# Kernel tuning notes

Hardware: AMD Instinct MI355X
Metric: run time of the kernel (lower is better)

## Reference

```python
import jax, jax.numpy as jnp
import numpy as np

B, S, IN, HID = 8, 2048, 1024, 1024

def setup_inputs() -> dict:
    key = jax.random.key(0)
    ks = jax.random.split(key, 6)
    scale = 1.0 / np.sqrt(IN + HID)
    return {
        "x": jax.random.normal(ks[0], (B, S, IN), dtype=jnp.float32),
        "h": jax.random.normal(ks[1], (B, S, HID), dtype=jnp.float32),
        "W1": jax.random.normal(ks[2], (HID, IN + HID), dtype=jnp.float32) * scale,
        "b1": jax.random.normal(ks[3], (HID,), dtype=jnp.float32) * scale,
        "W2": jax.random.normal(ks[4], (HID, IN + HID), dtype=jnp.float32) * scale,
        "b2": jax.random.normal(ks[5], (HID,), dtype=jnp.float32) * scale,
    }

def reference(x, h, W1, b1, W2, b2):
    # combined1 = cat(x, h) ; forget = sigmoid(Linear1(combined1))
    combined1 = jnp.concatenate((x, h), axis=2)          # [B,S,IN+HID]
    forget = jax.nn.sigmoid(jnp.einsum('bsf,hf->bsh', combined1, W1) + b1)
    interim_h = forget * h                                # [B,S,HID]
    combined2 = jnp.concatenate((x, interim_h), axis=2)   # [B,S,IN+HID]
    interim_o = jnp.tanh(jnp.einsum('bsf,hf->bsh', combined2, W2) + b2)
    output = (1.0 - forget) * h + forget * interim_o
    return (output, output)
```

## Files before the change

### kernel.cpp

```cpp
#include <hip/hip_runtime.h>
#include <stdint.h>


#define M_ROWS 16384
#define K_DIM  2048
#define N_DIM  1024

typedef float  f32x4  __attribute__((ext_vector_type(4)));
typedef __bf16 bf16x8 __attribute__((ext_vector_type(8)));
typedef unsigned short u16x8 __attribute__((ext_vector_type(8)));

typedef __attribute__((address_space(3))) void as3_void;
typedef __attribute__((address_space(1))) void as1_void;

__device__ __forceinline__ void gload_lds16(const unsigned short* g, void* lds) {
    __builtin_amdgcn_global_load_lds((const as1_void*)g, (as3_void*)lds, 16, 0, 0);
}

__device__ __forceinline__ unsigned short f2bf(float f) {
    union { float f; unsigned u; } v; v.f = f;
    unsigned r = 0x7FFFu + ((v.u >> 16) & 1u);
    return (unsigned short)((v.u + r) >> 16);
}


__global__ void pack_A(const float* __restrict__ x, const float* __restrict__ h,
                       unsigned short* __restrict__ Abf) {
    size_t t = (size_t)blockIdx.x * blockDim.x + threadIdx.x;
    size_t e = t * 8;
    int row = (int)(e >> 11);
    int col = (int)(e & 2047);
    const float* src = (col < 1024) ? (x + (size_t)row * 1024 + col)
                                    : (h + (size_t)row * 1024 + (col - 1024));
    f32x4 v0 = ((const f32x4*)src)[0];
    f32x4 v1 = ((const f32x4*)src)[1];
    u16x8 o;
    o[0] = f2bf(v0[0]); o[1] = f2bf(v0[1]); o[2] = f2bf(v0[2]); o[3] = f2bf(v0[3]);
    o[4] = f2bf(v1[0]); o[5] = f2bf(v1[1]); o[6] = f2bf(v1[2]); o[7] = f2bf(v1[3]);
    *(u16x8*)(Abf + e) = o;
}

__global__ void pack_W(const float* __restrict__ W1, const float* __restrict__ W2,
                       unsigned short* __restrict__ W1b, unsigned short* __restrict__ W2b) {
    size_t t = (size_t)blockIdx.x * blockDim.x + threadIdx.x;
    size_t e = t * 8;
    int which = (int)(e >> 21);
    size_t e2 = e & ((1u << 21) - 1);
    const float* src = (which ? W2 : W1) + e2;
    unsigned short* dst = (which ? W2b : W1b) + e2;
    f32x4 v0 = ((const f32x4*)src)[0];
    f32x4 v1 = ((const f32x4*)src)[1];
    u16x8 o;
    o[0] = f2bf(v0[0]); o[1] = f2bf(v0[1]); o[2] = f2bf(v0[2]); o[3] = f2bf(v0[3]);
    o[4] = f2bf(v1[0]); o[5] = f2bf(v1[1]); o[6] = f2bf(v1[2]); o[7] = f2bf(v1[3]);
    *(u16x8*)dst = o;
}


#define NT (K_DIM / 32)

__global__ __launch_bounds__(256) void gemm1(
        const unsigned short* __restrict__ Abf,
        const unsigned short* __restrict__ Wb,
        const float* __restrict__ bias,
        const float* __restrict__ h,
        float* Fout,
        unsigned short* __restrict__ H2)
{
    __shared__ unsigned short As[2][4096];
    __shared__ unsigned short Bs[2][4096];

    int bid = blockIdx.x;
    int tn = bid & 7, tm = bid >> 3;
    int m0 = tm * 128, n0 = tn * 128;

    int t = threadIdx.x, wave = t >> 6;
    int lane = t & 63;
    int wr = wave >> 1, wc = wave & 1;
    int fr = lane & 15, fq = lane >> 4;
    int sRow = t >> 2, sCol = (t & 3) * 8;

    const unsigned short* aBase = Abf + (size_t)(m0 + sRow) * K_DIM + sCol;
    const unsigned short* bBase = Wb  + (size_t)(n0 + sRow) * K_DIM + sCol;
    int ldsW = wave * 1024;

#define STAGE1(bufi, k0s)                                              \
    do {                                                               \
        char* AsB = (char*)As[bufi];  char* BsB = (char*)Bs[bufi];     \
        gload_lds16(aBase + (k0s),                AsB + ldsW);         \
        gload_lds16(aBase + 64 * K_DIM + (k0s),   AsB + 4096 + ldsW);  \
        gload_lds16(bBase + (k0s),                BsB + ldsW);         \
        gload_lds16(bBase + 64 * K_DIM + (k0s),   BsB + 4096 + ldsW);  \
    } while (0)

    f32x4 acc[4][4] = {};

    STAGE1(0, 0);
    __syncthreads();

    int cur = 0;
    for (int ti = 0; ti < NT; ++ti) {
        if (ti + 1 < NT) STAGE1(cur ^ 1, (ti + 1) * 32);
        bf16x8 af[4], bfr[4];
#pragma unroll
        for (int i = 0; i < 4; i++) {
            af[i]  = *(const bf16x8*)&As[cur][(wr * 64 + i * 16 + fr) * 32 + fq * 8];
            bfr[i] = *(const bf16x8*)&Bs[cur][(wc * 64 + i * 16 + fr) * 32 + fq * 8];
        }
        __builtin_amdgcn_s_setprio(1);
#pragma unroll
        for (int mi = 0; mi < 4; mi++)
#pragma unroll
            for (int ni = 0; ni < 4; ni++)
                acc[mi][ni] = __builtin_amdgcn_mfma_f32_16x16x32_bf16(
                                  af[mi], bfr[ni], acc[mi][ni], 0, 0, 0);
        __builtin_amdgcn_s_setprio(0);
        __syncthreads();
        cur ^= 1;
    }
#undef STAGE1

    int rowBase = m0 + wr * 64 + fq * 4;
    int colBase = n0 + wc * 64 + fr;
#pragma unroll
    for (int mi = 0; mi < 4; mi++) {
#pragma unroll
        for (int ni = 0; ni < 4; ni++) {
            int col = colBase + ni * 16;
            float b = bias[col];
#pragma unroll
            for (int j = 0; j < 4; j++) {
                int row = rowBase + mi * 16 + j;
                size_t idx = (size_t)row * N_DIM + col;
                float c = acc[mi][ni][j] + b;
                float f = 1.0f / (1.0f + expf(-c));
                Fout[idx] = f;
                float hv = h[idx];
                H2[idx] = f2bf(f * hv);
            }
        }
    }
}

__global__ __launch_bounds__(256) void gemm2(
        const unsigned short* __restrict__ Abf,
        const unsigned short* __restrict__ H2,
        const unsigned short* __restrict__ Wb,
        const float* __restrict__ bias,
        const float* __restrict__ h,
        float* Fout,
        float* Out2)
{
    __shared__ unsigned short As[2][4096];
    __shared__ unsigned short Bs[2][4096];

    int bid = blockIdx.x;
    int tn = bid & 7, tm = bid >> 3;
    int m0 = tm * 128, n0 = tn * 128;

    int t = threadIdx.x, wave = t >> 6;
    int lane = t & 63;
    int wr = wave >> 1, wc = wave & 1;
    int fr = lane & 15, fq = lane >> 4;
    int sRow = t >> 2, sCol = (t & 3) * 8;

    const unsigned short* aBase1 = Abf + (size_t)(m0 + sRow) * K_DIM + sCol;
    const unsigned short* aBase2 = H2  + (size_t)(m0 + sRow) * N_DIM + sCol;
    const unsigned short* bBase  = Wb  + (size_t)(n0 + sRow) * K_DIM + sCol;
    int ldsW = wave * 1024;

#define STAGE2(bufi, k0s)                                                   \
    do {                                                                    \
        char* AsB = (char*)As[bufi];  char* BsB = (char*)Bs[bufi];          \
        if ((k0s) < 1024) {                                                 \
            gload_lds16(aBase1 + (k0s),               AsB + ldsW);          \
            gload_lds16(aBase1 + 64 * K_DIM + (k0s),  AsB + 4096 + ldsW);   \
        } else {                                                            \
            int kk = (k0s) - 1024;                                          \
            gload_lds16(aBase2 + kk,                  AsB + ldsW);          \
            gload_lds16(aBase2 + 64 * N_DIM + kk,     AsB + 4096 + ldsW);   \
        }                                                                   \
        gload_lds16(bBase + (k0s),                BsB + ldsW);              \
        gload_lds16(bBase + 64 * K_DIM + (k0s),   BsB + 4096 + ldsW);       \
    } while (0)

    f32x4 acc[4][4] = {};

    STAGE2(0, 0);
    __syncthreads();

    int cur = 0;
    for (int ti = 0; ti < NT; ++ti) {
        if (ti + 1 < NT) STAGE2(cur ^ 1, (ti + 1) * 32);
        bf16x8 af[4], bfr[4];
#pragma unroll
        for (int i = 0; i < 4; i++) {
            af[i]  = *(const bf16x8*)&As[cur][(wr * 64 + i * 16 + fr) * 32 + fq * 8];
            bfr[i] = *(const bf16x8*)&Bs[cur][(wc * 64 + i * 16 + fr) * 32 + fq * 8];
        }
        __builtin_amdgcn_s_setprio(1);
#pragma unroll
        for (int mi = 0; mi < 4; mi++)
#pragma unroll
            for (int ni = 0; ni < 4; ni++)
                acc[mi][ni] = __builtin_amdgcn_mfma_f32_16x16x32_bf16(
                                  af[mi], bfr[ni], acc[mi][ni], 0, 0, 0);
        __builtin_amdgcn_s_setprio(0);
        __syncthreads();
        cur ^= 1;
    }
#undef STAGE2

    int rowBase = m0 + wr * 64 + fq * 4;
    int colBase = n0 + wc * 64 + fr;
#pragma unroll
    for (int mi = 0; mi < 4; mi++) {
#pragma unroll
        for (int ni = 0; ni < 4; ni++) {
            int col = colBase + ni * 16;
            float b = bias[col];
#pragma unroll
            for (int j = 0; j < 4; j++) {
                int row = rowBase + mi * 16 + j;
                size_t idx = (size_t)row * N_DIM + col;
                float c = acc[mi][ni][j] + b;
                float o = tanhf(c);
                float f = Fout[idx];
                float hv = h[idx];
                float out = fmaf(f, o - hv, hv);
                Fout[idx] = out;
                Out2[idx] = out;
            }
        }
    }
}


extern "C" void kernel_launch(void* const* d_in, const int* in_sizes, int n_in,
                              void* d_out, int out_size, void* d_ws, size_t ws_size,
                              hipStream_t stream) {
    const float* x  = (const float*)d_in[0];
    const float* h  = (const float*)d_in[1];
    const float* W1 = (const float*)d_in[2];
    const float* b1 = (const float*)d_in[3];
    const float* W2 = (const float*)d_in[4];
    const float* b2 = (const float*)d_in[5];
    float* out = (float*)d_out;
    float* out2 = out + (size_t)M_ROWS * N_DIM;

    unsigned short* Abf = (unsigned short*)d_ws;
    unsigned short* H2  = (unsigned short*)((char*)d_ws + 67108864);
    unsigned short* W1b = (unsigned short*)((char*)d_ws + 100663296);
    unsigned short* W2b = (unsigned short*)((char*)d_ws + 104857600);

    pack_A<<<16384, 256, 0, stream>>>(x, h, Abf);
    pack_W<<<2048, 256, 0, stream>>>(W1, W2, W1b, W2b);
    gemm1<<<1024, 256, 0, stream>>>(Abf, W1b, b1, h, out, H2);
    gemm2<<<1024, 256, 0, stream>>>(Abf, H2, W2b, b2, h, out, out2);
}
```

Measured before the change: 577.3 us.

## Triple-buffer LDS loads with one barrier per iteration and remap block order

Both GEMM kernels go from double-buffered to triple-buffered LDS staging, prefetching two tiles ahead. They now use explicit vmcnt waits and a single barrier per K-step instead of two __syncthreads. Block IDs are also remapped so that consecutive blocks share the same N tile and walk along M, which changes L2 reuse of the weight tile versus the A rows. This raises LDS use per block and could lower occupancy. It also relies on hand-written waitcnt counts that must match the number of global_load_lds calls issued.

```diff
diff --git a/kernel.cpp b/kernel.cpp
--- a/kernel.cpp
+++ b/kernel.cpp
@@ -67,21 +67,21 @@
         float* Fout,
         unsigned short* __restrict__ H2)
 {
-    __shared__ unsigned short As[2][4096];
-    __shared__ unsigned short Bs[2][4096];
+    __shared__ unsigned short As[3][4096];
+    __shared__ unsigned short Bs[3][4096];
 
     int bid = blockIdx.x;
-    int tn = bid & 7, tm = bid >> 3;
+    int wg  = (bid & 7) * 128 + (bid >> 3);
+    int tn = wg & 7, tm = wg >> 3;
     int m0 = tm * 128, n0 = tn * 128;
 
     int t = threadIdx.x, wave = t >> 6;
     int lane = t & 63;
     int wr = wave >> 1, wc = wave & 1;
     int fr = lane & 15, fq = lane >> 4;
-    int sRow = t >> 2, sCol = (t & 3) * 8;
-
-    const unsigned short* aBase = Abf + (size_t)(m0 + sRow) * K_DIM + sCol;
-    const unsigned short* bBase = Wb  + (size_t)(n0 + sRow) * K_DIM + sCol;
+
+    const unsigned short* aBase = Abf + (size_t)(m0 + (t >> 2)) * K_DIM + (t & 3) * 8;
+    const unsigned short* bBase = Wb  + (size_t)(n0 + (t >> 2)) * K_DIM + (t & 3) * 8;
     int ldsW = wave * 1024;
 
 #define STAGE1(bufi, k0s)                                              \
@@ -96,11 +96,19 @@
     f32x4 acc[4][4] = {};
 
     STAGE1(0, 0);
-    __syncthreads();
-
+    STAGE1(1, 32);
     int cur = 0;
     for (int ti = 0; ti < NT; ++ti) {
-        if (ti + 1 < NT) STAGE1(cur ^ 1, (ti + 1) * 32);
+        if (ti + 1 < NT) {
+            asm volatile("s_waitcnt vmcnt(4)" ::: "memory");
+        } else {
+            asm volatile("s_waitcnt vmcnt(0)" ::: "memory");
+        }
+        __builtin_amdgcn_s_barrier();
+        if (ti + 2 < NT) {
+            int nb = cur + 2; if (nb >= 3) nb -= 3;
+            STAGE1(nb, (ti + 2) * 32);
+        }
         bf16x8 af[4], bfr[4];
 #pragma unroll
         for (int i = 0; i < 4; i++) {
@@ -115,8 +123,7 @@
                 acc[mi][ni] = __builtin_amdgcn_mfma_f32_16x16x32_bf16(
                                   af[mi], bfr[ni], acc[mi][ni], 0, 0, 0);
         __builtin_amdgcn_s_setprio(0);
-        __syncthreads();
-        cur ^= 1;
+        cur = (cur == 2) ? 0 : cur + 1;
     }
 #undef STAGE1
 
@@ -151,22 +158,22 @@
         float* Fout,
         float* Out2)
 {
-    __shared__ unsigned short As[2][4096];
-    __shared__ unsigned short Bs[2][4096];
+    __shared__ unsigned short As[3][4096];
+    __shared__ unsigned short Bs[3][4096];
 
     int bid = blockIdx.x;
-    int tn = bid & 7, tm = bid >> 3;
+    int wg  = (bid & 7) * 128 + (bid >> 3);
+    int tn = wg & 7, tm = wg >> 3;
     int m0 = tm * 128, n0 = tn * 128;
 
     int t = threadIdx.x, wave = t >> 6;
     int lane = t & 63;
     int wr = wave >> 1, wc = wave & 1;
     int fr = lane & 15, fq = lane >> 4;
-    int sRow = t >> 2, sCol = (t & 3) * 8;
-
-    const unsigned short* aBase1 = Abf + (size_t)(m0 + sRow) * K_DIM + sCol;
-    const unsigned short* aBase2 = H2  + (size_t)(m0 + sRow) * N_DIM + sCol;
-    const unsigned short* bBase  = Wb  + (size_t)(n0 + sRow) * K_DIM + sCol;
+
+    const unsigned short* aBase1 = Abf + (size_t)(m0 + (t >> 2)) * K_DIM + (t & 3) * 8;
+    const unsigned short* aBase2 = H2  + (size_t)(m0 + (t >> 2)) * N_DIM + (t & 3) * 8;
+    const unsigned short* bBase  = Wb  + (size_t)(n0 + (t >> 2)) * K_DIM + (t & 3) * 8;
     int ldsW = wave * 1024;
 
 #define STAGE2(bufi, k0s)                                                   \
@@ -187,11 +194,19 @@
     f32x4 acc[4][4] = {};
 
     STAGE2(0, 0);
-    __syncthreads();
-
+    STAGE2(1, 32);
     int cur = 0;
     for (int ti = 0; ti < NT; ++ti) {
-        if (ti + 1 < NT) STAGE2(cur ^ 1, (ti + 1) * 32);
+        if (ti + 1 < NT) {
+            asm volatile("s_waitcnt vmcnt(4)" ::: "memory");
+        } else {
+            asm volatile("s_waitcnt vmcnt(0)" ::: "memory");
+        }
+        __builtin_amdgcn_s_barrier();
+        if (ti + 2 < NT) {
+            int nb = cur + 2; if (nb >= 3) nb -= 3;
+            STAGE2(nb, (ti + 2) * 32);
+        }
         bf16x8 af[4], bfr[4];
 #pragma unroll
         for (int i = 0; i < 4; i++) {
@@ -206,8 +221,7 @@
                 acc[mi][ni] = __builtin_amdgcn_mfma_f32_16x16x32_bf16(
                                   af[mi], bfr[ni], acc[mi][ni], 0, 0, 0);
         __builtin_amdgcn_s_setprio(0);
-        __syncthreads();
-        cur ^= 1;
+        cur = (cur == 2) ? 0 : cur + 1;
     }
 #undef STAGE2
 
```

Result: faster. 557.1 us (-3.5%).
